# Performance work log

Hardware: AMD Instinct MI355X
Metric: run time of the kernel (lower is better)

Reference implementation:

```python
import jax, jax.numpy as jnp
import numpy as np

TAU = 1.5
K = 4
EPS = 1e-5
GN_GROUPS = 8

def conv2d(x, w, pad, rhs_dilation=(1, 1)):
    return jax.lax.conv_general_dilated(
        x, w, window_strides=(1, 1),
        padding=[(pad, pad), (pad, pad)],
        rhs_dilation=rhs_dilation,
        dimension_numbers=("NCHW", "OIHW", "NCHW"))

def setup_inputs() -> dict:
    key = jax.random.key(0)
    ks = jax.random.split(key, 16)
    s = 0.05  # weight scale to keep activations sane
    B, C, H, W = 16, 128, 64, 64
    O, HID, CG, SE = 128, 32, 16, 16
    d = {}
    d["x"] = jax.random.normal(ks[0], (B, C, H, W), jnp.float32)
    d["base_weight"] = jax.random.normal(ks[1], (O, C, 3, 3), jnp.float32) * s
    d["delta_weight"] = jax.random.normal(ks[2], (K, O, C, 3, 3), jnp.float32) * s
    d["kernel_scale"] = jnp.ones((K, O, 1, 1, 1), jnp.float32)
    d["gc_w1"] = jax.random.normal(ks[3], (HID, C), jnp.float32) * s
    d["gc_w2"] = jax.random.normal(ks[4], (C, HID), jnp.float32) * s
    d["rc_w"] = jax.random.normal(ks[5], (HID, C, 3, 3), jnp.float32) * s
    d["bn_gamma"] = jnp.ones((HID,), jnp.float32)
    d["bn_beta"] = jnp.zeros((HID,), jnp.float32)
    d["bn_mean"] = jnp.zeros((HID,), jnp.float32)
    d["bn_var"] = jnp.ones((HID,), jnp.float32)
    d["rg_w"] = jax.random.normal(ks[6], (HID, C), jnp.float32) * s
    d["gate_w"] = jax.random.normal(ks[7], (K * O, HID), jnp.float32) * s
    d["gate_b"] = jnp.zeros((K * O,), jnp.float32)
    d["cg_w1"] = jax.random.normal(ks[8], (CG, C), jnp.float32) * s
    d["cg_b1"] = jnp.zeros((CG,), jnp.float32)
    d["cg_w2"] = jax.random.normal(ks[9], (C, CG), jnp.float32) * s
    d["cg_b2"] = jnp.zeros((C,), jnp.float32)
    d["sg_w"] = jax.random.normal(ks[10], (1, 2, 7, 7), jnp.float32) * s
    d["gn_gamma"] = jnp.ones((O,), jnp.float32)
    d["gn_beta"] = jnp.zeros((O,), jnp.float32)
    d["se_w1"] = jax.random.normal(ks[11], (SE, O), jnp.float32) * s
    d["se_b1"] = jnp.zeros((SE,), jnp.float32)
    d["se_w2"] = jax.random.normal(ks[12], (O, SE), jnp.float32) * s
    d["se_b2"] = jnp.zeros((O,), jnp.float32)
    d["identity_scale"] = jnp.float32(0.0)
    d["bias"] = jnp.zeros((O,), jnp.float32)
    return d

def reference(x, base_weight, delta_weight, kernel_scale, gc_w1, gc_w2, rc_w,
              bn_gamma, bn_beta, bn_mean, bn_var, rg_w, gate_w, gate_b,
              cg_w1, cg_b1, cg_w2, cg_b2, sg_w, gn_gamma, gn_beta,
              se_w1, se_b1, se_w2, se_b2, identity_scale, bias):
    identity = x
    B, C, H, W = x.shape
    O = base_weight.shape[0]

    # global context gate (squeeze-excite style)
    p = x.mean((2, 3))                                    # [B,C]
    g = jax.nn.sigmoid(jax.nn.silu(p @ gc_w1.T) @ gc_w2.T)
    x = x * g[:, :, None, None]

    # channel gate
    pc = x.mean((2, 3))
    c_attn = jax.nn.sigmoid(jax.nn.silu(pc @ cg_w1.T + cg_b1) @ cg_w2.T + cg_b2)
    # spatial gate
    s_in = jnp.concatenate([x.mean(1, keepdims=True), x.max(1, keepdims=True)], axis=1)
    s_attn = jax.nn.sigmoid(conv2d(s_in, sg_w, pad=3))
    x = x * c_attn[:, :, None, None] * s_attn

    # router: dilated conv + BN(eval) + SiLU, plus global branch
    lf = conv2d(x, rc_w, pad=2, rhs_dilation=(2, 2))
    lf = (lf - bn_mean[None, :, None, None]) * jax.lax.rsqrt(bn_var + EPS)[None, :, None, None]
    lf = lf * bn_gamma[None, :, None, None] + bn_beta[None, :, None, None]
    lf = jax.nn.silu(lf)
    gf = jax.nn.silu(x.mean((2, 3)) @ rg_w.T)             # [B,HID]
    lf = lf + gf[:, :, None, None]
    alpha = jnp.einsum("bhij,oh->boij", lf, gate_w) + gate_b[None, :, None, None]
    alpha = alpha.reshape(B, K, O, H, W)
    alpha = jax.nn.softmax(alpha / TAU, axis=1)

    # unfold (k=3, stride=1, pad=1, dilation=1) -> H_out=H, W_out=W
    xp = jnp.pad(x, ((0, 0), (0, 0), (1, 1), (1, 1)))
    patches = jnp.stack([xp[:, :, i:i + H, j:j + W]
                         for i in range(3) for j in range(3)], axis=2)  # [B,C,9,H,W]
    L = H * W
    xu = patches.reshape(B, C * 9, L).transpose(0, 2, 1)  # [B,L,C*9]

    base = base_weight.reshape(O, -1)
    delta = (delta_weight * kernel_scale).reshape(K, O, -1)
    # same-size bilinear resize of alpha is the identity
    alpha_map = alpha.reshape(B, K, O, L)

    static = jnp.einsum("blf,of->bol", xu, base)          # [B,O,L]
    res = jnp.einsum("blf,kof->bkol", xu, delta)          # [B,K,O,L]
    final = static + (res * alpha_map).sum(1)
    out = final.reshape(B, O, H, W)

    # GroupNorm
    go = out.reshape(B, GN_GROUPS, O // GN_GROUPS, H, W)
    mu = go.mean((2, 3, 4), keepdims=True)
    var = go.var((2, 3, 4), keepdims=True)
    out = ((go - mu) * jax.lax.rsqrt(var + EPS)).reshape(B, O, H, W)
    out = out * gn_gamma[None, :, None, None] + gn_beta[None, :, None, None]

    # output SE
    ps = out.mean((2, 3))
    se = jax.nn.sigmoid(jax.nn.silu(ps @ se_w1.T + se_b1) @ se_w2.T + se_b2)
    out = out * se[:, :, None, None]

    out = out + jnp.tanh(identity_scale) * identity
    out = out + bias[None, :, None, None]
    return out
```

## Files before the change

### kernel.cpp

```cpp
#include <hip/hip_runtime.h>
#include <hip/hip_bf16.h>
#include <math.h>

typedef __bf16 bf16_t;
typedef __bf16 bf16x8 __attribute__((ext_vector_type(8)));
typedef __bf16 bf16x4 __attribute__((ext_vector_type(4)));
typedef float  f32x4  __attribute__((ext_vector_type(4)));

#define EPSF 1e-5f
#define TAUF 1.5f

__device__ __forceinline__ float sigmoidf_(float x){ return 1.f/(1.f+__expf(-x)); }
__device__ __forceinline__ float siluf_(float x){ return x*sigmoidf_(x); }

__device__ __forceinline__ void gload_lds16(const void* g, void* l){
  __builtin_amdgcn_global_load_lds((const __attribute__((address_space(1))) unsigned int*)g,
                                   (__attribute__((address_space(3))) unsigned int*)l, 16, 0, 0);
}

__global__ void k_prep(const float* __restrict__ base_w, const float* __restrict__ delta_w,
                       const float* __restrict__ kscale, const float* __restrict__ rc_w,
                       bf16_t* __restrict__ WCQ, bf16_t* __restrict__ RCWQ,
                       bf16_t* __restrict__ x2q,
                       const float* __restrict__ x, float* __restrict__ p,
                       float* __restrict__ zbase){
  int bx = blockIdx.x;
  if (bx >= 4752){
    float4 z = {0.f,0.f,0.f,0.f};
    for (int i = threadIdx.x; i < 1536; i += 256)
      *(float4*)(zbase + i*4) = z;
    return;
  }
  if (bx >= 2704){
    int bc = bx - 2704; const float* xr = x + (size_t)bc*4096;
    float s = 0.f;
    for (int i = threadIdx.x; i < 4096; i += 256) s += xr[i];
    __shared__ float sb[4];
    for (int off=32; off; off>>=1) s += __shfl_down(s, off);
    if ((threadIdx.x & 63)==0) sb[threadIdx.x>>6] = s;
    __syncthreads();
    if (threadIdx.x==0) p[bc] = (sb[0]+sb[1]+sb[2]+sb[3]) * (1.f/4096.f);
    return;
  }
  if (bx >= 2448){
    int pp = bx - 2448;
    size_t base = (size_t)pp*68*68*8;
    float4 z = {0.f,0.f,0.f,0.f};
    for (int i = threadIdx.x; i < 272; i += 256){
      int r = i/68; int wp = i - r*68;
      int hp = (r&1) + (r>>1)*66;
      *(float4*)(x2q + base + ((size_t)hp*68 + wp)*8) = z;
    }
    {
      int i = threadIdx.x;
      int hp = 2 + (i>>2);
      int wp = (i&1) + (i&2)*33;
      *(float4*)(x2q + base + ((size_t)hp*68 + wp)*8) = z;
    }
    return;
  }
  int i = bx*256 + threadIdx.x;
  if (i < 589824){
    int c8 = i&7; int o16 = (i>>3)&15; int q = (i>>7)&3; int s = (i>>9)&3;
    int h2 = (i>>11)&3; int r = i>>13; int t = r%9; int ob = r/9;
    int o = ob*16 + o16; int c = h2*32 + q*8 + c8;
    float v = base_w[(o*128+c)*9 + t] + delta_w[(((s*128)+o)*128 + c)*9 + t]*kscale[s*128+o];
    WCQ[i] = (bf16_t)v;
  } else if (i < 589824 + 36864){
    int j = i - 589824;
    int c8 = j&7; int h16 = (j>>3)&15; int q = (j>>7)&3; int n2 = (j>>9)&1;
    int r = j>>10; int t = r%9; int h2 = r/9;
    int hid = n2*16 + h16; int c = h2*32 + q*8 + c8;
    RCWQ[j] = (bf16_t)rc_w[(hid*128+c)*9 + t];
  }
}

__global__ void k_spatial(const float* __restrict__ x, const float* __restrict__ p,
                          const float* __restrict__ gc_w1, const float* __restrict__ gc_w2,
                          float* __restrict__ sin_){
  int bi = blockIdx.x; int b = bi>>6; int h = bi&63;
  int tid = threadIdx.x, wv = tid>>6, w = tid&63;
  __shared__ float psum[4][64], pmax[4][64];
  __shared__ float ps[128], h1[32], gsh[128];
  if (tid < 128) ps[tid] = p[b*128+tid];
  __syncthreads();
  if (tid < 32){ float a=0.f; for(int c=0;c<128;c++) a += ps[c]*gc_w1[tid*128+c]; h1[tid]=siluf_(a); }
  __syncthreads();
  if (tid < 128){ float a=0.f; for(int j=0;j<32;j++) a += h1[j]*gc_w2[tid*32+j]; gsh[tid]=sigmoidf_(a); }
  __syncthreads();
  float sm=0.f, mx=-1e30f;
  const float* xb = x + (((size_t)b*128 + wv*32)*64 + h)*64 + w;
  #pragma unroll 4
  for (int c=0;c<32;c++){
    float v = xb[(size_t)c*4096] * gsh[wv*32+c];
    sm += v; mx = fmaxf(mx, v);
  }
  psum[wv][w]=sm; pmax[wv][w]=mx;
  __syncthreads();
  if (tid < 64){
    float s = psum[0][w]+psum[1][w]+psum[2][w]+psum[3][w];
    float m = fmaxf(fmaxf(pmax[0][w],pmax[1][w]),fmaxf(pmax[2][w],pmax[3][w]));
    sin_[b*8192 + h*64 + w]        = s*(1.f/128.f);
    sin_[b*8192 + 4096 + h*64 + w] = m;
  }
}

__global__ void __launch_bounds__(256) k_x2(
    const float* __restrict__ x, const float* __restrict__ p,
    const float* __restrict__ gc_w1, const float* __restrict__ gc_w2,
    const float* __restrict__ cg_w1, const float* __restrict__ cg_b1,
    const float* __restrict__ cg_w2, const float* __restrict__ cg_b2,
    const float* __restrict__ sin_, const float* __restrict__ sg_w,
    bf16_t* __restrict__ x2q, float* __restrict__ pc2){
  int bi = blockIdx.x; int b = bi>>6; int h = bi&63;
  __shared__ float tile[128*65];
  __shared__ float sh_sin[980];
  __shared__ float sh_sgw[98];
  __shared__ float satt_row[64];
  __shared__ float ps[128], h1[32], gsh[128], pcs[128], c1[16], gate_sh[128];
  int tid = threadIdx.x, wv = tid>>6, lane = tid&63;
  for (int i=tid;i<980;i+=256){
    int c2 = i/490; int rr = i - c2*490; int r = rr/70; int k = rr - r*70;
    int hh = h + r - 3; int ww = k - 3;
    float v = 0.f;
    if (hh>=0 && hh<64 && ww>=0 && ww<64) v = sin_[b*8192 + c2*4096 + hh*64 + ww];
    sh_sin[i] = v;
  }
  if (tid < 98) sh_sgw[tid] = sg_w[tid];
  if (tid < 128) ps[tid] = p[b*128+tid];
  __syncthreads();
  if (tid < 32){
    float a=0.f; for(int c=0;c<128;c++) a += ps[c]*gc_w1[tid*128+c]; h1[tid]=siluf_(a);
  } else if (tid >= 128 && tid < 192){
    int col = tid - 128;
    float a = 0.f;
    #pragma unroll
    for (int c2=0;c2<2;c2++)
      #pragma unroll
      for (int r=0;r<7;r++)
        #pragma unroll
        for (int j=0;j<7;j++)
          a += sh_sin[c2*490 + r*70 + col + j] * sh_sgw[c2*49 + r*7 + j];
    satt_row[col] = sigmoidf_(a);
  }
  __syncthreads();
  if (tid < 128){
    float a=0.f; for(int j=0;j<32;j++) a += h1[j]*gc_w2[tid*32+j];
    float g = sigmoidf_(a);
    gsh[tid] = g; pcs[tid] = ps[tid]*g;
  }
  __syncthreads();
  if (tid < 16){
    float a2=cg_b1[tid]; for(int c=0;c<128;c++) a2 += pcs[c]*cg_w1[tid*128+c]; c1[tid]=siluf_(a2);
  }
  __syncthreads();
  if (tid < 128){
    float a3=cg_b2[tid]; for(int j=0;j<16;j++) a3 += c1[j]*cg_w2[tid*16+j];
    gate_sh[tid] = gsh[tid]*sigmoidf_(a3);
  }
  __syncthreads();
  float sa = satt_row[lane];
  const float* xb = x + (((size_t)b*128 + wv*32)*64 + h)*64 + lane;
  #pragma unroll 8
  for (int i=0;i<32;i++)
    tile[(wv*32+i)*65 + lane] = xb[(size_t)i*4096] * gate_sh[wv*32+i] * sa;
  __syncthreads();
  for (int it=0; it<4; it++){
    int idx = it*256 + tid;
    int cq = idx>>6; int w = idx&63;
    int c0 = cq*8;
    bf16x8 v;
    #pragma unroll
    for (int e=0;e<8;e++) v[e] = (bf16_t)tile[(c0+e)*65 + w];
    *(bf16x8*)(x2q + (((((size_t)b*4 + (cq>>2))*4 + (cq&3))*68 + (h+2))*68 + (w+2))*8) = v;
  }
  if (tid < 128){
    const float* row = &tile[tid*65];
    float s = 0.f;
    #pragma unroll 8
    for (int w=0;w<64;w++) s += row[w];
    atomicAdd(&pc2[b*128+tid], s);
  }
}

__global__ void __launch_bounds__(256) k_router(
    const bf16_t* __restrict__ x2q, const bf16_t* __restrict__ RCWQ,
    const float* __restrict__ bn_gamma, const float* __restrict__ bn_beta,
    const float* __restrict__ bn_mean, const float* __restrict__ bn_var,
    const float* __restrict__ pc2, const float* __restrict__ rg_w,
    bf16_t* __restrict__ lfb){
  __shared__ __align__(16) char smem[44544];
  __shared__ float sgf[32];
  __shared__ float spart[256];
  int tid = threadIdx.x;
  int wv = tid>>6, lane = tid&63, m16 = lane&15, q = lane>>4;
  int rb = blockIdx.x & 31, b = blockIdx.x >> 5;
  int r0 = rb*2;
  int rloc = wv&1;
  int ws0 = (wv>>1)*2;

  {
    int hid = tid&31, seg = tid>>5;
    float a=0.f;
    #pragma unroll
    for (int j=0;j<16;j++) a += pc2[b*128 + seg*16 + j]*rg_w[hid*128 + seg*16 + j];
    spart[tid] = a;
  }

  f32x4 acc[2][2] = {};

  #pragma unroll 1
  for (int h2=0; h2<4; h2++){
    const char* asrc = (const char*)(x2q + ((((size_t)(b*4+h2)*4 + wv)*68 + r0)*68)*8);
    #pragma unroll
    for (int j=0;j<7;j++){
      if (j*64 + lane < 408)
        gload_lds16(asrc + j*1024 + lane*16, (char*)smem + wv*6528 + j*1024);
    }
    const char* wsrc = (const char*)(RCWQ + (size_t)h2*9216) + wv*4608;
    #pragma unroll
    for (int j=0;j<5;j++){
      if (j*64 + lane < 288)
        gload_lds16(wsrc + j*1024 + lane*16, (char*)smem + 26112 + wv*4608 + j*1024);
    }
    __syncthreads();
    if (h2==0 && tid < 32){
      float s = 0.f;
      #pragma unroll
      for (int k=0;k<8;k++) s += spart[k*32+tid];
      sgf[tid] = siluf_(s*(1.f/4096.f));
    }
    #pragma unroll
    for (int t=0; t<9; t++){
      int di = t/3, dj = t - di*3;
      bf16x8 aw0 = *(const bf16x8*)((const char*)smem + 26112 + (t*2+0)*1024 + q*256 + m16*16);
      bf16x8 aw1 = *(const bf16x8*)((const char*)smem + 26112 + (t*2+1)*1024 + q*256 + m16*16);
      #pragma unroll
      for (int mt=0; mt<2; mt++){
        int wseg = ws0 + mt;
        bf16x8 bs = *(const bf16x8*)((const char*)smem + q*6528 +
                     ((rloc + 2*di)*68 + wseg*16 + m16 + 2*dj)*16);
        acc[0][mt] = __builtin_amdgcn_mfma_f32_16x16x32_bf16(aw0, bs, acc[0][mt], 0,0,0);
        acc[1][mt] = __builtin_amdgcn_mfma_f32_16x16x32_bf16(aw1, bs, acc[1][mt], 0,0,0);
      }
    }
    __syncthreads();
  }

  #pragma unroll
  for (int n2=0;n2<2;n2++){
    float aa[4], bb[4];
    #pragma unroll
    for (int i=0;i<4;i++){
      int hid = n2*16 + q*4 + i;
      float a = bn_gamma[hid]*rsqrtf(bn_var[hid]+EPSF);
      aa[i] = a;
      bb[i] = bn_beta[hid] - bn_mean[hid]*a;
    }
    #pragma unroll
    for (int mt=0;mt<2;mt++){
      bf16x4 yv;
      #pragma unroll
      for (int i=0;i<4;i++){
        int hid = n2*16 + q*4 + i;
        yv[i] = (bf16_t)(siluf_(aa[i]*acc[n2][mt][i] + bb[i]) + sgf[hid]);
      }
      size_t pos = (size_t)b*4096 + (r0+rloc)*64 + (ws0+mt)*16 + m16;
      *(bf16x4*)(lfb + pos*32 + n2*16 + q*4) = yv;
    }
  }
}

__global__ void __launch_bounds__(512, 2) k_main(
    const bf16_t* __restrict__ x2q, const bf16_t* __restrict__ WCQ,
    const bf16_t* __restrict__ lfb, const float* __restrict__ gate_w,
    const float* __restrict__ gate_b, bf16_t* __restrict__ outp,
    float* __restrict__ csum, float* __restrict__ cssq){
  __shared__ __align__(16) char smem[161920];
  float* sred = (float*)(smem + 160896);

  int tid = threadIdx.x;
  int wv = tid>>6, lane = tid&63, m16 = lane&15, q = lane>>4;
  int hf = wv>>2, w4 = wv&3;
  int bx = blockIdx.x;
  int ob2 = bx >> 7; int rem = bx & 127; int b = rem >> 3; int hb = rem & 7;
  int h0 = hb*8;
  int obase = (ob2*2 + hf)*16;

  auto STAGE_A = [&](int h2, int bsel){
    int quad = wv>>1, rh = wv&1;
    const char* asrc = (const char*)(x2q + ((((size_t)(b*4+h2)*4 + quad)*68 + (h0+1+rh*5))*68)*8);
    char* adst = (char*)smem + bsel*43584 + quad*10896 + rh*5440;
    #pragma unroll
    for (int j=0;j<6;j++){
      if (j*64 + lane < 340)
        gload_lds16(asrc + (j*64+lane)*16, adst + j*1024);
    }
  };
  auto STAGE_B = [&](int h2){
    int obh = ob2*2 + hf;
    const char* wsrc = (const char*)WCQ + (size_t)(obh*9*4 + h2)*4096;
    char* bdst = (char*)smem + 87168 + hf*36864 + w4*9216;
    #pragma unroll
    for (int j=0;j<9;j++){
      int cc = w4*576 + j*64 + lane;
      int tap = cc>>8, r = cc&255;
      gload_lds16(wsrc + tap*16384 + r*16, bdst + j*1024);
    }
  };

  f32x4 acc[8][4] = {};

  int baseA[8];
  #pragma unroll
  for (int mi=0;mi<8;mi++){
    int row = w4*2 + (mi>>2); int wseg = mi&3;
    baseA[mi] = q*10896 + (row*68 + wseg*16 + m16 + 1)*16;
  }
  int baseB = q*256 + m16*16;

  STAGE_A(0, 0);
  STAGE_B(0);

  #pragma unroll 1
  for (int h2=0; h2<4; h2++){
    if (h2 < 3){
      STAGE_A(h2+1, (h2+1)&1);
      asm volatile("s_waitcnt vmcnt(6)" ::: "memory");
    } else {
      asm volatile("s_waitcnt vmcnt(0)" ::: "memory");
    }
    __builtin_amdgcn_s_barrier();

    const char* Ab = (const char*)smem + (h2&1)*43584;
    const char* Bb = (const char*)smem + 87168 + hf*36864;
    #pragma unroll
    for (int t=0; t<9; t++){
      int di = t/3, dj = t - di*3;
      int toff = (di*68 + dj)*16;
      bf16x8 av[8], bv[4];
      #pragma unroll
      for (int mi=0;mi<8;mi++) av[mi] = *(const bf16x8*)(Ab + baseA[mi] + toff);
      #pragma unroll
      for (int s=0;s<4;s++)  bv[s] = *(const bf16x8*)(Bb + t*4096 + s*1024 + baseB);
      #pragma unroll
      for (int s=0;s<4;s++){
        #pragma unroll
        for (int mi=0;mi<8;mi++)
          acc[mi][s] = __builtin_amdgcn_mfma_f32_16x16x32_bf16(av[mi], bv[s], acc[mi][s], 0,0,0);
      }
    }
    __builtin_amdgcn_s_barrier();
    if (h2 < 3) STAGE_B(h2+1);
  }

  const char* lfsrc = (const char*)(lfb + ((size_t)b*4096 + h0*64)*32);
  #pragma unroll
  for (int j=0;j<4;j++)
    gload_lds16(lfsrc + j*8192 + wv*1024 + lane*16, (char*)smem + j*8192 + wv*1024);
  bf16_t* shGW = (bf16_t*)(smem + 32768);
  for (int idx = tid; idx < 4096; idx += 512){
    int hf2 = idx>>11; int n = (idx>>5)&63; int j2 = idx&31;
    shGW[idx] = (bf16_t)gate_w[((n>>4)*128 + (ob2*2+hf2)*16 + (n&15))*32 + j2];
  }
  __syncthreads();

  bf16x8 bg[4];
  #pragma unroll
  for (int kk=0;kk<4;kk++)
    bg[kk] = *(const bf16x8*)((const char*)shGW + hf*4096 + (kk*16+m16)*64 + q*16);
  float gb[4];
  #pragma unroll
  for (int kk=0;kk<4;kk++) gb[kk] = gate_b[kk*128 + obase + m16];

  const float itau = 1.f/TAUF;
  float s1 = 0.f, s2 = 0.f;
  size_t orow = ((size_t)(b*128 + obase + m16))*4096 + h0*64;
  #pragma unroll
  for (int mi=0; mi<8; mi++){
    bf16x8 avL = *(const bf16x8*)((const char*)smem + (w4*128 + mi*16 + m16)*64 + q*16);
    f32x4 zero = {};
    f32x4 lg[4];
    #pragma unroll
    for (int kk=0;kk<4;kk++)
      lg[kk] = __builtin_amdgcn_mfma_f32_16x16x32_bf16(avL, bg[kk], zero, 0,0,0);
    bf16x4 yv;
    #pragma unroll
    for (int r=0;r<4;r++){
      float l0 = (lg[0][r]+gb[0])*itau, l1 = (lg[1][r]+gb[1])*itau;
      float l2 = (lg[2][r]+gb[2])*itau, l3 = (lg[3][r]+gb[3])*itau;
      float mx = fmaxf(fmaxf(l0,l1),fmaxf(l2,l3));
      float e0=__expf(l0-mx), e1=__expf(l1-mx), e2=__expf(l2-mx), e3=__expf(l3-mx);
      float inv = 1.f/(e0+e1+e2+e3);
      float y = (e0*acc[mi][0][r] + e1*acc[mi][1][r]
               + e2*acc[mi][2][r] + e3*acc[mi][3][r])*inv;
      s1 += y; s2 += y*y;
      yv[r] = (bf16_t)y;
    }
    *(bf16x4*)(outp + orow + w4*128 + mi*16 + q*4) = yv;
  }

  s1 += __shfl_down(s1, 32); s1 += __shfl_down(s1, 16);
  s2 += __shfl_down(s2, 32); s2 += __shfl_down(s2, 16);
  if (lane < 16){ sred[wv*16 + lane] = s1; sred[128 + wv*16 + lane] = s2; }
  __syncthreads();
  if (tid < 32){
    int hf2 = tid>>4, o = tid&15;
    float a = 0.f, c = 0.f;
    #pragma unroll
    for (int k=0;k<4;k++){
      a += sred[(hf2*4+k)*16 + o];
      c += sred[128 + (hf2*4+k)*16 + o];
    }
    atomicAdd(&csum[b*128 + (ob2*2+hf2)*16 + o], a);
    atomicAdd(&cssq[b*128 + (ob2*2+hf2)*16 + o], c);
  }
}

__global__ void __launch_bounds__(256) k_final(
    const bf16_t* __restrict__ outp, const float* __restrict__ x,
    const float* __restrict__ csum, const float* __restrict__ cssq,
    const float* __restrict__ gn_gamma, const float* __restrict__ gn_beta,
    const float* __restrict__ se_w1, const float* __restrict__ se_b1,
    const float* __restrict__ se_w2, const float* __restrict__ se_b2,
    const float* __restrict__ bias, const float* __restrict__ iscale,
    float* __restrict__ out){
  int bo = blockIdx.x; int b = bo>>7; int o = bo&127;
  int tid = threadIdx.x;
  __shared__ float s1[128], s2[128], gmu[8], grs[8], psl[128], t1[16], scb[2];
  if (tid < 128){ s1[tid] = csum[b*128+tid]; s2[tid] = cssq[b*128+tid]; }
  __syncthreads();
  if (tid < 8){
    float a=0.f,a2=0.f; for(int j=0;j<16;j++){ a+=s1[tid*16+j]; a2+=s2[tid*16+j]; }
    float mu = a*(1.f/65536.f); float var = a2*(1.f/65536.f) - mu*mu;
    gmu[tid]=mu; grs[tid]=rsqrtf(var+EPSF);
  }
  __syncthreads();
  if (tid < 128){
    int g = tid>>4;
    psl[tid] = (s1[tid]*(1.f/4096.f) - gmu[g])*grs[g]*gn_gamma[tid] + gn_beta[tid];
  }
  __syncthreads();
  if (tid < 16){ float a = se_b1[tid]; for(int c=0;c<128;c++) a += psl[c]*se_w1[tid*128+c]; t1[tid]=siluf_(a); }
  __syncthreads();
  if (tid == 0){
    float a = se_b2[o]; for(int j=0;j<16;j++) a += t1[j]*se_w2[o*16+j];
    float sev = sigmoidf_(a); int g = o>>4;
    scb[0] = grs[g]*gn_gamma[o]*sev;
    scb[1] = (gn_beta[o] - gmu[g]*grs[g]*gn_gamma[o])*sev;
  }
  __syncthreads();
  float ts = tanhf(iscale[0]);
  float A = scb[0], Bv = scb[1] + bias[o];
  size_t base = (size_t)bo*4096 + tid*16;
  #pragma unroll
  for (int hh=0; hh<2; hh++){
    size_t i = base + hh*8;
    bf16x8 ov = *(const bf16x8*)(outp + i);
    float4 x0 = *(const float4*)(x+i), x1 = *(const float4*)(x+i+4);
    float4 r0, r1;
    r0.x = (float)ov[0]*A + Bv + ts*x0.x;
    r0.y = (float)ov[1]*A + Bv + ts*x0.y;
    r0.z = (float)ov[2]*A + Bv + ts*x0.z;
    r0.w = (float)ov[3]*A + Bv + ts*x0.w;
    r1.x = (float)ov[4]*A + Bv + ts*x1.x;
    r1.y = (float)ov[5]*A + Bv + ts*x1.y;
    r1.z = (float)ov[6]*A + Bv + ts*x1.z;
    r1.w = (float)ov[7]*A + Bv + ts*x1.w;
    *(float4*)(out+i) = r0; *(float4*)(out+i+4) = r1;
  }
}

extern "C" void kernel_launch(void* const* d_in, const int* in_sizes, int n_in,
                              void* d_out, int out_size, void* d_ws, size_t ws_size,
                              hipStream_t stream){
  const float* x      = (const float*)d_in[0];
  const float* base_w = (const float*)d_in[1];
  const float* delta_w= (const float*)d_in[2];
  const float* kscale = (const float*)d_in[3];
  const float* gc_w1  = (const float*)d_in[4];
  const float* gc_w2  = (const float*)d_in[5];
  const float* rc_w   = (const float*)d_in[6];
  const float* bn_g   = (const float*)d_in[7];
  const float* bn_b   = (const float*)d_in[8];
  const float* bn_m   = (const float*)d_in[9];
  const float* bn_v   = (const float*)d_in[10];
  const float* rg_w   = (const float*)d_in[11];
  const float* gate_w = (const float*)d_in[12];
  const float* gate_b = (const float*)d_in[13];
  const float* cg_w1  = (const float*)d_in[14];
  const float* cg_b1  = (const float*)d_in[15];
  const float* cg_w2  = (const float*)d_in[16];
  const float* cg_b2  = (const float*)d_in[17];
  const float* sg_w   = (const float*)d_in[18];
  const float* gn_g   = (const float*)d_in[19];
  const float* gn_b   = (const float*)d_in[20];
  const float* se_w1  = (const float*)d_in[21];
  const float* se_b1  = (const float*)d_in[22];
  const float* se_w2  = (const float*)d_in[23];
  const float* se_b2  = (const float*)d_in[24];
  const float* iscale = (const float*)d_in[25];
  const float* bias   = (const float*)d_in[26];
  float* out = (float*)d_out;

  char* ws = (char*)d_ws;
  size_t off = 0;
  auto alloc = [&](size_t bytes)->void*{ void* p = ws + off; off += (bytes + 255) & ~(size_t)255; return p; };
  bf16_t* X2Q = (bf16_t*)alloc(16ull*4*4*68*68*8*2);
  bf16_t* WCQ = (bf16_t*)alloc(589824ull*2);
  bf16_t* RCWQ= (bf16_t*)alloc(36864ull*2);
  bf16_t* LF  = (bf16_t*)alloc(16ull*4096*32*2);
  bf16_t* OUTP= (bf16_t*)alloc(16ull*128*4096*2);
  float* PC2  = (float*)alloc(2048*4);
  float* CSUM = (float*)alloc(2048*4);
  float* CSSQ = (float*)alloc(2048*4);
  float* P    = (float*)alloc(2048*4);
  float* SIN  = (float*)alloc(16ull*8192*4);

  k_prep   <<<4753, 256, 0, stream>>>(base_w, delta_w, kscale, rc_w, WCQ, RCWQ, X2Q, x, P, PC2);
  k_spatial<<<1024, 256, 0, stream>>>(x, P, gc_w1, gc_w2, SIN);
  k_x2     <<<1024, 256, 0, stream>>>(x, P, gc_w1, gc_w2, cg_w1, cg_b1, cg_w2, cg_b2, SIN, sg_w, X2Q, PC2);
  k_router <<<512,  256, 0, stream>>>(X2Q, RCWQ, bn_g, bn_b, bn_m, bn_v, PC2, rg_w, LF);
  k_main   <<<512,  512, 0, stream>>>(X2Q, WCQ, LF, gate_w, gate_b, OUTP, CSUM, CSSQ);
  k_final  <<<2048, 256, 0, stream>>>(OUTP, x, CSUM, CSSQ, gn_g, gn_b, se_w1, se_b1, se_w2, se_b2, bias, iscale, out);
}
```

Before: 266.9 us.

## Split weight staging into two tap groups to overlap loads with MFMA

```diff
diff --git a/kernel.cpp b/kernel.cpp
--- a/kernel.cpp
+++ b/kernel.cpp
@@ -297,13 +297,24 @@
         gload_lds16(asrc + (j*64+lane)*16, adst + j*1024);
     }
   };
-  auto STAGE_B = [&](int h2){
+  auto STAGE_B_G0 = [&](int h2){
     int obh = ob2*2 + hf;
     const char* wsrc = (const char*)WCQ + (size_t)(obh*9*4 + h2)*4096;
-    char* bdst = (char*)smem + 87168 + hf*36864 + w4*9216;
-    #pragma unroll
-    for (int j=0;j<9;j++){
-      int cc = w4*576 + j*64 + lane;
+    char* bdst = (char*)smem + 87168 + hf*36864 + w4*5120;
+    #pragma unroll
+    for (int j=0;j<5;j++){
+      int cc = w4*320 + j*64 + lane;
+      int tap = cc>>8, r = cc&255;
+      gload_lds16(wsrc + tap*16384 + r*16, bdst + j*1024);
+    }
+  };
+  auto STAGE_B_G1 = [&](int h2){
+    int obh = ob2*2 + hf;
+    const char* wsrc = (const char*)WCQ + (size_t)(obh*9*4 + h2)*4096;
+    char* bdst = (char*)smem + 87168 + hf*36864 + 20480 + w4*4096;
+    #pragma unroll
+    for (int j=0;j<4;j++){
+      int cc = 1280 + w4*256 + j*64 + lane;
       int tap = cc>>8, r = cc&255;
       gload_lds16(wsrc + tap*16384 + r*16, bdst + j*1024);
     }
@@ -320,22 +331,20 @@
   int baseB = q*256 + m16*16;
 
   STAGE_A(0, 0);
-  STAGE_B(0);
+  STAGE_B_G0(0);
 
   #pragma unroll 1
   for (int h2=0; h2<4; h2++){
-    if (h2 < 3){
-      STAGE_A(h2+1, (h2+1)&1);
-      asm volatile("s_waitcnt vmcnt(6)" ::: "memory");
-    } else {
-      asm volatile("s_waitcnt vmcnt(0)" ::: "memory");
-    }
+    STAGE_B_G1(h2);
+    if (h2 < 3) STAGE_A(h2+1, (h2+1)&1);
+    if (h2 < 3) asm volatile("s_waitcnt vmcnt(10)" ::: "memory");
+    else        asm volatile("s_waitcnt vmcnt(4)"  ::: "memory");
     __builtin_amdgcn_s_barrier();
 
     const char* Ab = (const char*)smem + (h2&1)*43584;
     const char* Bb = (const char*)smem + 87168 + hf*36864;
     #pragma unroll
-    for (int t=0; t<9; t++){
+    for (int t=0; t<5; t++){
       int di = t/3, dj = t - di*3;
       int toff = (di*68 + dj)*16;
       bf16x8 av[8], bv[4];
@@ -350,14 +359,36 @@
           acc[mi][s] = __builtin_amdgcn_mfma_f32_16x16x32_bf16(av[mi], bv[s], acc[mi][s], 0,0,0);
       }
     }
+    if (h2 < 3) asm volatile("s_waitcnt vmcnt(6)" ::: "memory");
+    else        asm volatile("s_waitcnt vmcnt(0)" ::: "memory");
     __builtin_amdgcn_s_barrier();
-    if (h2 < 3) STAGE_B(h2+1);
-  }
-
-  const char* lfsrc = (const char*)(lfb + ((size_t)b*4096 + h0*64)*32);
-  #pragma unroll
-  for (int j=0;j<4;j++)
-    gload_lds16(lfsrc + j*8192 + wv*1024 + lane*16, (char*)smem + j*8192 + wv*1024);
+    if (h2 < 3){
+      STAGE_B_G0(h2+1);
+    } else {
+      const char* lfsrc = (const char*)(lfb + ((size_t)b*4096 + h0*64)*32);
+      #pragma unroll
+      for (int j=0;j<4;j++)
+        gload_lds16(lfsrc + j*8192 + wv*1024 + lane*16, (char*)smem + j*8192 + wv*1024);
+    }
+    #pragma unroll
+    for (int t=5; t<9; t++){
+      int di = t/3, dj = t - di*3;
+      int toff = (di*68 + dj)*16;
+      bf16x8 av[8], bv[4];
+      #pragma unroll
+      for (int mi=0;mi<8;mi++) av[mi] = *(const bf16x8*)(Ab + baseA[mi] + toff);
+      #pragma unroll
+      for (int s=0;s<4;s++)  bv[s] = *(const bf16x8*)(Bb + t*4096 + s*1024 + baseB);
+      #pragma unroll
+      for (int s=0;s<4;s++){
+        #pragma unroll
+        for (int mi=0;mi<8;mi++)
+          acc[mi][s] = __builtin_amdgcn_mfma_f32_16x16x32_bf16(av[mi], bv[s], acc[mi][s], 0,0,0);
+      }
+    }
+    __builtin_amdgcn_s_barrier();
+  }
+
   bf16_t* shGW = (bf16_t*)(smem + 32768);
   for (int idx = tid; idx < 4096; idx += 512){
     int hf2 = idx>>11; int n = (idx>>5)&63; int j2 = idx&31;
```

After: 272.1 us. Within noise of the previous version (+1.9%).
